# Performance work log

Hardware: AMD Instinct MI355X
Metric: run time of the kernel (lower is better)

The kernel has to match this reference:

```python
import jax, jax.numpy as jnp
import numpy as np

K = 4096   # infeatures (k)
N = 4096   # outfeatures (n)
G = 128    # quantization groupsize
M = 8192   # tokens (batch*seq)


def setup_inputs() -> dict:
    key = jax.random.key(0)
    kA, kB, kS = jax.random.split(key, 3)
    A = jax.random.normal(kA, (M, K), dtype=jnp.float32)
    # Packed int4 weights: each int32 holds 8 consecutive nibbles along k.
    B = jax.random.randint(kB, (K // 8, N), 0, 2**31 - 1, dtype=jnp.int32)
    # Per-group symmetric scales, positive and small like real quant scales.
    s = jax.random.uniform(kS, (K // G, N), dtype=jnp.float32) * 0.02 + 0.005
    return {"A": A, "B": B, "s": s}


def dequant(B, s):
    """Unpack int4 nibbles, center by 8 (symmetric zero-point), apply per-group scales.
    B: (K//8, N) int32 -> returns (K, N) float weight matrix."""
    shifts = (jnp.arange(8, dtype=jnp.int32) * 4)
    nib = (B[:, None, :] >> shifts[None, :, None]) & 0xF       # (K//8, 8, N) in [0,15]
    w = nib.reshape(B.shape[0] * 8, B.shape[1]).astype(s.dtype) - 8.0  # (K, N)
    scale = jnp.repeat(s, w.shape[0] // s.shape[0], axis=0)    # (K, N) group-broadcast
    return w * scale


def reference(A, B, s):
    # C = A @ dequant(B, s): fused int4-dequant GEMM (Marlin forward math).
    return A @ dequant(B, s)
```

## Files before the change

kernel.cpp:

```cpp
#include <hip/hip_runtime.h>
#include <hip/hip_fp16.h>


constexpr int MDIM = 8192;
constexpr int NDIM = 4096;
constexpr int KDIM = 4096;
constexpr int BM = 128;
constexpr int BN = 128;
constexpr int BK = 64;
constexpr int THREADS = 256;
constexpr int KSTEPS = KDIM / BK;

typedef _Float16 f16x8 __attribute__((ext_vector_type(8)));
typedef float f32x4 __attribute__((ext_vector_type(4)));

__device__ __forceinline__ unsigned int pack_dq(unsigned int q, __half2 k1032,
                                                __half2 sh) {
  __half2 h = __builtin_bit_cast(__half2, q);
  h = __hmul2(__hsub2(h, k1032), sh);
  return __builtin_bit_cast(unsigned int, h);
}

__device__ __forceinline__ unsigned int cvt2(float lo, float hi) {
  auto p = __builtin_amdgcn_cvt_pkrtz(lo, hi);
  return __builtin_bit_cast(unsigned int, p);
}

__global__ __launch_bounds__(THREADS, 2)
void marlin_fused(const float* __restrict__ A, const int* __restrict__ Bq,
                  const float* __restrict__ S, float* __restrict__ C) {
  __shared__ char lds[(BM * BK + BN * BK) * 2];
  char* As = lds;
  char* Bs = lds + BM * BK * 2;

  const int tid  = threadIdx.x;
  const int lane = tid & 63;
  const int wave = tid >> 6;
  const int wm = (wave >> 1) * 64;
  const int wn = (wave & 1) * 64;

  const int per = gridDim.x >> 3;
  const int b   = blockIdx.x;
  const int swz = (b & 7) * per + (b >> 3);
  const int nt  = swz & 31;
  const int mt  = swz >> 5;
  const int row0 = mt * BM;
  const int col0 = nt * BN;

  f32x4 acc[4][4];
#pragma unroll
  for (int i = 0; i < 4; ++i)
#pragma unroll
    for (int j = 0; j < 4; ++j)
      acc[i][j] = f32x4{0.f, 0.f, 0.f, 0.f};

  const int ar = tid >> 3;
  const int ac = tid & 7;
  const float* a_src = A + (size_t)(row0 + ar) * KDIM + ac * 8;
  const int a_off0 = (ar * 128 + ac * 16) ^ ((ar & 7) << 4);

  const int kp = tid >> 5;
  const int nl = (tid & 31) * 4;
  const int* b_src = Bq + (size_t)kp * NDIM + col0 + nl;
  const float* s_src = S + col0 + nl;
  int bofs[4];
#pragma unroll
  for (int j = 0; j < 4; ++j) {
    const int r = nl + j;
    bofs[j] = (r * 128 + kp * 16) ^ ((((r & 7) ^ ((r >> 3) & 3))) << 4);
  }

  const int swzr = (lane & 7) << 4;
  const int arow = wm + (lane & 15);
  const int brow = wn + (lane & 15);
  const int kofs = (lane >> 4) << 4;

  float4 av[4][2];
  int4 bv;
  float4 sv;

  auto load_tile = [&](int kt) {
#pragma unroll
    for (int i = 0; i < 4; ++i) {
      const float* src = a_src + (size_t)i * 32 * KDIM + kt * BK;
      av[i][0] = *reinterpret_cast<const float4*>(src);
      av[i][1] = *reinterpret_cast<const float4*>(src + 4);
    }
    bv = *reinterpret_cast<const int4*>(b_src + (size_t)kt * 8 * NDIM);
    sv = *reinterpret_cast<const float4*>(s_src + (size_t)(kt >> 1) * NDIM);
  };

  auto stage_tile = [&]() {
#pragma unroll
    for (int i = 0; i < 4; ++i) {
      uint4 w;
      w.x = cvt2(av[i][0].x, av[i][1].x);
      w.y = cvt2(av[i][0].y, av[i][1].y);
      w.z = cvt2(av[i][0].z, av[i][1].z);
      w.w = cvt2(av[i][0].w, av[i][1].w);
      *reinterpret_cast<uint4*>(As + a_off0 + i * 32 * 128) = w;
    }
    const __half2 k1032 = __float2half2_rn(1032.0f);
    const int bw[4] = {bv.x, bv.y, bv.z, bv.w};
    const float sc[4] = {sv.x, sv.y, sv.z, sv.w};
#pragma unroll
    for (int j = 0; j < 4; ++j) {
      const unsigned int ub = (unsigned int)bw[j];
      const unsigned int m4 = 0x000F000Fu, e10 = 0x64006400u;
      const __half2 sh = __float2half2_rn(sc[j]);
      uint4 w;
      w.x = pack_dq((ub & m4) | e10, k1032, sh);
      w.y = pack_dq(((ub >> 4) & m4) | e10, k1032, sh);
      w.z = pack_dq(((ub >> 8) & m4) | e10, k1032, sh);
      w.w = pack_dq(((ub >> 12) & m4) | e10, k1032, sh);
      *reinterpret_cast<uint4*>(Bs + bofs[j]) = w;
    }
  };

  auto compute_tile = [&]() {
#pragma unroll
    for (int ks = 0; ks < 2; ++ks) {
      f16x8 af[4], bf[4];
#pragma unroll
      for (int mi = 0; mi < 4; ++mi) {
        const int o = ((arow + mi * 16) * 128 + ks * 64 + kofs) ^ swzr;
        af[mi] = *reinterpret_cast<const f16x8*>(As + o);
      }
#pragma unroll
      for (int ni = 0; ni < 4; ++ni) {
        const int r = brow + ni * 16;
        const int o = (r * 128 + ks * 64 + kofs) ^
                      ((((r & 7) ^ ((r >> 3) & 3))) << 4);
        bf[ni] = *reinterpret_cast<const f16x8*>(Bs + o);
      }
#pragma unroll
      for (int mi = 0; mi < 4; ++mi)
#pragma unroll
        for (int ni = 0; ni < 4; ++ni)
          acc[mi][ni] = __builtin_amdgcn_mfma_f32_16x16x32_f16(
              af[mi], bf[ni], acc[mi][ni], 0, 0, 0);
    }
  };

  load_tile(0);
  stage_tile();
  __syncthreads();
#pragma unroll 1
  for (int kt = 0; kt < KSTEPS; ++kt) {
    const bool has_next = (kt + 1) < KSTEPS;
    if (has_next) load_tile(kt + 1);
    compute_tile();
    if (has_next) {
      __syncthreads();
      stage_tile();
      __syncthreads();
    }
  }

  const int crow = (lane >> 4) << 2;
  const int ccol = lane & 15;
#pragma unroll
  for (int mi = 0; mi < 4; ++mi)
#pragma unroll
    for (int ni = 0; ni < 4; ++ni) {
      const size_t base = (size_t)(row0 + wm + mi * 16 + crow) * NDIM
                          + (size_t)(col0 + wn + ni * 16 + ccol);
#pragma unroll
      for (int r = 0; r < 4; ++r)
        C[base + (size_t)r * NDIM] = acc[mi][ni][r];
    }
}

extern "C" void kernel_launch(void* const* d_in, const int* in_sizes, int n_in,
                              void* d_out, int out_size, void* d_ws, size_t ws_size,
                              hipStream_t stream) {
  (void)in_sizes; (void)n_in; (void)d_ws; (void)ws_size; (void)out_size;
  const float* A = (const float*)d_in[0];
  const int* Bq  = (const int*)d_in[1];
  const float* S = (const float*)d_in[2];
  float* C = (float*)d_out;
  const int grid = (MDIM / BM) * (NDIM / BN);
  marlin_fused<<<grid, THREADS, 0, stream>>>(A, Bq, S, C);
}
```

Before: 540.4 us.

## Double-buffer LDS tiles to halve barriers per k-step

Allocates two LDS buffers for the A and B tiles and alternates between them, unrolling the k-loop by two. Staging of the next tile into the other buffer happens before computing on the current one, so only one barrier per k-step is needed instead of two. LDS usage doubles per block, which could affect occupancy with two blocks per CU.

```diff
diff --git a/kernel.cpp b/kernel.cpp
--- a/kernel.cpp
+++ b/kernel.cpp
@@ -10,6 +10,8 @@
 constexpr int BK = 64;
 constexpr int THREADS = 256;
 constexpr int KSTEPS = KDIM / BK;
+constexpr int ABYTES = BM * BK * 2;
+constexpr int BBYTES = BN * BK * 2;
 
 typedef _Float16 f16x8 __attribute__((ext_vector_type(8)));
 typedef float f32x4 __attribute__((ext_vector_type(4)));
@@ -29,9 +31,11 @@
 __global__ __launch_bounds__(THREADS, 2)
 void marlin_fused(const float* __restrict__ A, const int* __restrict__ Bq,
                   const float* __restrict__ S, float* __restrict__ C) {
-  __shared__ char lds[(BM * BK + BN * BK) * 2];
-  char* As = lds;
-  char* Bs = lds + BM * BK * 2;
+  __shared__ char lds[2 * (ABYTES + BBYTES)];
+  char* const As0 = lds;
+  char* const Bs0 = lds + ABYTES;
+  char* const As1 = lds + ABYTES + BBYTES;
+  char* const Bs1 = lds + 2 * ABYTES + BBYTES;
 
   const int tid  = threadIdx.x;
   const int lane = tid & 63;
@@ -90,7 +94,7 @@
     sv = *reinterpret_cast<const float4*>(s_src + (size_t)(kt >> 1) * NDIM);
   };
 
-  auto stage_tile = [&]() {
+  auto stage_tile = [&](char* As, char* Bs) {
 #pragma unroll
     for (int i = 0; i < 4; ++i) {
       uint4 w;
@@ -117,7 +121,7 @@
     }
   };
 
-  auto compute_tile = [&]() {
+  auto compute_tile = [&](const char* As, const char* Bs) {
 #pragma unroll
     for (int ks = 0; ks < 2; ++ks) {
       f16x8 af[4], bf[4];
@@ -143,19 +147,27 @@
   };
 
   load_tile(0);
-  stage_tile();
+  stage_tile(As0, Bs0);
+  load_tile(1);
   __syncthreads();
+
 #pragma unroll 1
-  for (int kt = 0; kt < KSTEPS; ++kt) {
-    const bool has_next = (kt + 1) < KSTEPS;
-    if (has_next) load_tile(kt + 1);
-    compute_tile();
-    if (has_next) {
-      __syncthreads();
-      stage_tile();
-      __syncthreads();
-    }
+  for (int kt = 0; kt < KSTEPS - 2; kt += 2) {
+    stage_tile(As1, Bs1);
+    load_tile(kt + 2);
+    compute_tile(As0, Bs0);
+    __syncthreads();
+
+    stage_tile(As0, Bs0);
+    load_tile(kt + 3);
+    compute_tile(As1, Bs1);
+    __syncthreads();
   }
+
+  stage_tile(As1, Bs1);
+  compute_tile(As0, Bs0);
+  __syncthreads();
+  compute_tile(As1, Bs1);
 
   const int crow = (lane >> 4) << 2;
   const int ccol = lane & 15;
```

New measurement: 622.3 us. 15.1% more time.

## Split into A/B pre-conversion kernels and direct-to-LDS f16 GEMM

Applied to the files above, without the earlier changes.

Adds two prep kernels that convert A to fp16 and dequantize B into pre-swizzled tile-contiguous layouts in the workspace. A new GEMM kernel then streams those tiles straight into LDS with global_load_lds, so the main loop no longer converts or dequantizes in registers and can run at higher occupancy. The fallback fused kernel is also restructured without register prefetch. The cost is extra global traffic: fp16 A and B are written and read back once, plus two extra launches, and the new GEMM loop has no double buffering.

```diff
diff --git a/kernel.cpp b/kernel.cpp
--- a/kernel.cpp
+++ b/kernel.cpp
@@ -10,9 +10,16 @@
 constexpr int BK = 64;
 constexpr int THREADS = 256;
 constexpr int KSTEPS = KDIM / BK;
+constexpr int TILE_B = BM * BK * 2;
+constexpr int MT = MDIM / BM;
+constexpr int NT = NDIM / BN;
+constexpr size_t AH_BYTES = (size_t)MT * KSTEPS * TILE_B;
+constexpr size_t WT_BYTES = (size_t)NT * KSTEPS * TILE_B;
 
 typedef _Float16 f16x8 __attribute__((ext_vector_type(8)));
 typedef float f32x4 __attribute__((ext_vector_type(4)));
+typedef __attribute__((address_space(3))) unsigned int lds_u32;
+typedef const __attribute__((address_space(1))) unsigned int glb_u32;
 
 __device__ __forceinline__ unsigned int pack_dq(unsigned int q, __half2 k1032,
                                                 __half2 sh) {
@@ -26,12 +33,155 @@
   return __builtin_bit_cast(unsigned int, p);
 }
 
+
+__global__ __launch_bounds__(THREADS)
+void prep_a(const float* __restrict__ A, char* __restrict__ Ah) {
+  const int bid = blockIdx.x;
+  const int mt = bid >> 6, kt = bid & 63;
+  const int t = threadIdx.x;
+  const int ar = t >> 3;
+  const int ac = t & 7;
+  char* tile = Ah + (size_t)bid * TILE_B;
+#pragma unroll
+  for (int i = 0; i < 4; ++i) {
+    const int r = ar + 32 * i;
+    const float* src = A + (size_t)(mt * BM + r) * KDIM + kt * BK + ac * 8;
+    const float4 v0 = *reinterpret_cast<const float4*>(src);
+    const float4 v1 = *reinterpret_cast<const float4*>(src + 4);
+    uint4 w;
+    w.x = cvt2(v0.x, v1.x);
+    w.y = cvt2(v0.y, v1.y);
+    w.z = cvt2(v0.z, v1.z);
+    w.w = cvt2(v0.w, v1.w);
+    *reinterpret_cast<uint4*>(tile + ((r * 128 + ac * 16) ^ ((r & 7) << 4))) = w;
+  }
+}
+
+__global__ __launch_bounds__(THREADS)
+void prep_b(const int* __restrict__ Bq, const float* __restrict__ S,
+            char* __restrict__ Wt) {
+  const int bid = blockIdx.x;
+  const int nt = bid >> 6, kt = bid & 63;
+  const int t = threadIdx.x;
+  const int kp = t >> 5;
+  const int nl = (t & 31) * 4;
+  char* tile = Wt + (size_t)bid * TILE_B;
+  const int4 bv = *reinterpret_cast<const int4*>(
+      Bq + (size_t)(kt * 8 + kp) * NDIM + nt * BN + nl);
+  const float4 sv = *reinterpret_cast<const float4*>(
+      S + (size_t)(kt >> 1) * NDIM + nt * BN + nl);
+  const __half2 k1032 = __float2half2_rn(1032.0f);
+  const int bw[4] = {bv.x, bv.y, bv.z, bv.w};
+  const float sc[4] = {sv.x, sv.y, sv.z, sv.w};
+#pragma unroll
+  for (int j = 0; j < 4; ++j) {
+    const unsigned int ub = (unsigned int)bw[j];
+    const unsigned int m4 = 0x000F000Fu, e10 = 0x64006400u;
+    const __half2 sh = __float2half2_rn(sc[j]);
+    uint4 w;
+    w.x = pack_dq((ub & m4) | e10, k1032, sh);
+    w.y = pack_dq(((ub >> 4) & m4) | e10, k1032, sh);
+    w.z = pack_dq(((ub >> 8) & m4) | e10, k1032, sh);
+    w.w = pack_dq(((ub >> 12) & m4) | e10, k1032, sh);
+    const int r = nl + j;
+    *reinterpret_cast<uint4*>(tile + ((r * 128 + kp * 16) ^ ((r & 7) << 4))) = w;
+  }
+}
+
+
+__global__ __launch_bounds__(THREADS, 3)
+void gemm_f16(const char* __restrict__ Ah, const char* __restrict__ Wt,
+              float* __restrict__ C) {
+  __shared__ char lds[2 * TILE_B];
+  char* const As = lds;
+  char* const Bs = lds + TILE_B;
+
+  const int tid  = threadIdx.x;
+  const int lane = tid & 63;
+  const int wave = tid >> 6;
+  const int wm = (wave >> 1) * 64;
+  const int wn = (wave & 1) * 64;
+
+  const int per = gridDim.x >> 3;
+  const int b   = blockIdx.x;
+  const int swzb = (b & 7) * per + (b >> 3);
+  const int nt  = swzb & 31;
+  const int mt  = swzb >> 5;
+  const char* atiles = Ah + (size_t)mt * KSTEPS * TILE_B;
+  const char* btiles = Wt + (size_t)nt * KSTEPS * TILE_B;
+
+  f32x4 acc[4][4];
+#pragma unroll
+  for (int i = 0; i < 4; ++i)
+#pragma unroll
+    for (int j = 0; j < 4; ++j)
+      acc[i][j] = f32x4{0.f, 0.f, 0.f, 0.f};
+
+  const int swzr = (lane & 7) << 4;
+  const int arow = wm + (lane & 15);
+  const int brow = wn + (lane & 15);
+  const int kofs = (lane >> 4) << 4;
+  const int so   = wave * 1024 + lane * 16;
+  const int sd   = wave * 1024;
+
+#pragma unroll 1
+  for (int kt = 0; kt < KSTEPS; ++kt) {
+    const char* at = atiles + (size_t)kt * TILE_B;
+    const char* bt = btiles + (size_t)kt * TILE_B;
+#pragma unroll
+    for (int i = 0; i < 4; ++i) {
+      __builtin_amdgcn_global_load_lds((glb_u32*)(at + i * 4096 + so),
+                                       (lds_u32*)(As + i * 4096 + sd), 16, 0, 0);
+      __builtin_amdgcn_global_load_lds((glb_u32*)(bt + i * 4096 + so),
+                                       (lds_u32*)(Bs + i * 4096 + sd), 16, 0, 0);
+    }
+    __syncthreads();
+
+#pragma unroll
+    for (int ks = 0; ks < 2; ++ks) {
+      f16x8 af[4], bf[4];
+#pragma unroll
+      for (int mi = 0; mi < 4; ++mi) {
+        const int o = ((arow + mi * 16) * 128 + ks * 64 + kofs) ^ swzr;
+        af[mi] = *reinterpret_cast<const f16x8*>(As + o);
+      }
+#pragma unroll
+      for (int ni = 0; ni < 4; ++ni) {
+        const int o = ((brow + ni * 16) * 128 + ks * 64 + kofs) ^ swzr;
+        bf[ni] = *reinterpret_cast<const f16x8*>(Bs + o);
+      }
+#pragma unroll
+      for (int mi = 0; mi < 4; ++mi)
+#pragma unroll
+        for (int ni = 0; ni < 4; ++ni)
+          acc[mi][ni] = __builtin_amdgcn_mfma_f32_16x16x32_f16(
+              af[mi], bf[ni], acc[mi][ni], 0, 0, 0);
+    }
+    __syncthreads();
+  }
+
+  const int crow = (lane >> 4) << 2;
+  const int ccol = lane & 15;
+  const int row0 = mt * BM, col0 = nt * BN;
+#pragma unroll
+  for (int mi = 0; mi < 4; ++mi)
+#pragma unroll
+    for (int ni = 0; ni < 4; ++ni) {
+      const size_t base = (size_t)(row0 + wm + mi * 16 + crow) * NDIM
+                          + (size_t)(col0 + wn + ni * 16 + ccol);
+#pragma unroll
+      for (int r = 0; r < 4; ++r)
+        C[base + (size_t)r * NDIM] = acc[mi][ni][r];
+    }
+}
+
+
 __global__ __launch_bounds__(THREADS, 2)
 void marlin_fused(const float* __restrict__ A, const int* __restrict__ Bq,
                   const float* __restrict__ S, float* __restrict__ C) {
-  __shared__ char lds[(BM * BK + BN * BK) * 2];
+  __shared__ char lds[2 * TILE_B];
   char* As = lds;
-  char* Bs = lds + BM * BK * 2;
+  char* Bs = lds + TILE_B;
 
   const int tid  = threadIdx.x;
   const int lane = tid & 63;
@@ -142,19 +292,13 @@
     }
   };
 
-  load_tile(0);
-  stage_tile();
-  __syncthreads();
 #pragma unroll 1
   for (int kt = 0; kt < KSTEPS; ++kt) {
-    const bool has_next = (kt + 1) < KSTEPS;
-    if (has_next) load_tile(kt + 1);
+    load_tile(kt);
+    __syncthreads();
+    stage_tile();
+    __syncthreads();
     compute_tile();
-    if (has_next) {
-      __syncthreads();
-      stage_tile();
-      __syncthreads();
-    }
   }
 
   const int crow = (lane >> 4) << 2;
@@ -174,11 +318,20 @@
 extern "C" void kernel_launch(void* const* d_in, const int* in_sizes, int n_in,
                               void* d_out, int out_size, void* d_ws, size_t ws_size,
                               hipStream_t stream) {
-  (void)in_sizes; (void)n_in; (void)d_ws; (void)ws_size; (void)out_size;
+  (void)in_sizes; (void)n_in; (void)out_size;
   const float* A = (const float*)d_in[0];
   const int* Bq  = (const int*)d_in[1];
   const float* S = (const float*)d_in[2];
   float* C = (float*)d_out;
   const int grid = (MDIM / BM) * (NDIM / BN);
-  marlin_fused<<<grid, THREADS, 0, stream>>>(A, Bq, S, C);
-}
+
+  if (ws_size >= AH_BYTES + WT_BYTES) {
+    char* Ah = (char*)d_ws;
+    char* Wt = (char*)d_ws + AH_BYTES;
+    prep_a<<<MT * KSTEPS, THREADS, 0, stream>>>(A, Ah);
+    prep_b<<<NT * KSTEPS, THREADS, 0, stream>>>(Bq, S, Wt);
+    gemm_f16<<<grid, THREADS, 0, stream>>>(Ah, Wt, C);
+  } else {
+    marlin_fused<<<grid, THREADS, 0, stream>>>(A, Bq, S, C);
+  }
+}
```

Result: faster. 516.0 us (-4.5%).
